# Kernel tuning notes

Measured on AMD Instinct MI355X. Metric: run time of the kernel, lower is better.

The kernel has to match this reference:

```python
import jax, jax.numpy as jnp
import numpy as np

D_MODEL = 1024
NUM_HEADS = 16
HEAD_DIM = D_MODEL // NUM_HEADS


def setup_inputs() -> dict:
    key = jax.random.key(0)
    ks = jax.random.split(key, 7)
    B, S = 4, 2048
    scale = 1.0 / np.sqrt(D_MODEL)
    x = jax.random.normal(ks[0], (B, S, D_MODEL), dtype=jnp.float32)
    Wq = jax.random.normal(ks[1], (D_MODEL, D_MODEL), dtype=jnp.float32) * scale
    Wk = jax.random.normal(ks[2], (D_MODEL, D_MODEL), dtype=jnp.float32) * scale
    Wv = jax.random.normal(ks[3], (D_MODEL, D_MODEL), dtype=jnp.float32) * scale
    bq = jax.random.normal(ks[4], (D_MODEL,), dtype=jnp.float32) * 0.02
    bk = jax.random.normal(ks[5], (D_MODEL,), dtype=jnp.float32) * 0.02
    bv = jax.random.normal(ks[6], (D_MODEL,), dtype=jnp.float32) * 0.02
    return {"x": x, "Wq": Wq, "bq": bq, "Wk": Wk, "bk": bk, "Wv": Wv, "bv": bv}


def reference(x, Wq, bq, Wk, bk, Wv, bv):
    B, S, _ = x.shape
    # QKV projections (nn.Linear: x @ W^T + b; here W stored as [in, out] already)
    q = x @ Wq + bq
    k = x @ Wk + bk
    v = x @ Wv + bv
    # [B, H, S, Dh]
    def split_heads(t):
        return t.reshape(B, S, NUM_HEADS, HEAD_DIM).transpose(0, 2, 1, 3)
    q, k, v = split_heads(q), split_heads(k), split_heads(v)
    # NOTE: module scales by sqrt(d_model), NOT sqrt(head_dim)
    scores = jnp.einsum("bhqd,bhkd->bhqk", q, k) / jnp.sqrt(jnp.float32(D_MODEL))
    attn = jax.nn.softmax(scores, axis=-1)  # dropout = identity (eval mode)
    out = jnp.einsum("bhqk,bhkd->bhqd", attn, v)
    return out.transpose(0, 2, 1, 3).reshape(B, S, D_MODEL)
```

## Files before the change

kernel.cpp:

```cpp
#include <hip/hip_runtime.h>


typedef __attribute__((ext_vector_type(8))) __bf16 bf16x8;
typedef __attribute__((ext_vector_type(8))) unsigned short ushort8;
typedef __attribute__((ext_vector_type(4))) float floatx4;

#if __has_builtin(__builtin_amdgcn_exp2f)
#define EXP2(x) __builtin_amdgcn_exp2f(x)
#else
#define EXP2(x) __expf((x) * 0.6931471805599453f)
#endif

__device__ __forceinline__ unsigned short f2bf(float f) {
    __bf16 h = (__bf16)f;
    return __builtin_bit_cast(unsigned short, h);
}
__device__ __forceinline__ bf16x8 pack8(floatx4 a, floatx4 b) {
    bf16x8 v = {(__bf16)a[0], (__bf16)a[1], (__bf16)a[2], (__bf16)a[3],
                (__bf16)b[0], (__bf16)b[1], (__bf16)b[2], (__bf16)b[3]};
    return v;
}
__device__ __forceinline__ floatx4 mfma16(bf16x8 a, bf16x8 b, floatx4 c) {
    return __builtin_amdgcn_mfma_f32_16x16x32_bf16(a, b, c, 0, 0, 0);
}
__device__ __forceinline__ int spos(int s) {
    int rk = s & 31;
    return (s & ~31) | (((rk & 15) >> 2) * 8 + ((rk >> 4) << 2) + (rk & 3));
}
__device__ __forceinline__ void glds16(const void* g, void* l) {
    __builtin_amdgcn_global_load_lds(
        (const __attribute__((address_space(1))) unsigned int*)g,
        (__attribute__((address_space(3))) unsigned int*)l, 16, 0, 0);
}

__global__ __launch_bounds__(256) void prep_x(const float* __restrict__ X,
                                              unsigned short* __restrict__ Xb) {
    int i = (blockIdx.x * 256 + threadIdx.x) * 8;
    float4 a = *(const float4*)&X[i];
    float4 b = *(const float4*)&X[i + 4];
    bf16x8 v = {(__bf16)a.x, (__bf16)a.y, (__bf16)a.z, (__bf16)a.w,
                (__bf16)b.x, (__bf16)b.y, (__bf16)b.z, (__bf16)b.w};
    *(bf16x8*)&Xb[i] = v;
}

__global__ __launch_bounds__(256) void prep_wt(
    const float* __restrict__ Wq, const float* __restrict__ Wk,
    const float* __restrict__ Wv,
    unsigned short* __restrict__ WqT, unsigned short* __restrict__ WkT,
    unsigned short* __restrict__ WvT) {
    __shared__ unsigned short Ls[64 * 72];
    const int tid = threadIdx.x, z = blockIdx.z;
    const float* W = (z == 0) ? Wq : (z == 1) ? Wk : Wv;
    unsigned short* WT = (z == 0) ? WqT : (z == 1) ? WkT : WvT;
    const int k0 = (blockIdx.x >> 4) * 64, o0 = (blockIdx.x & 15) * 64;
#pragma unroll
    for (int e = 0; e < 4; ++e) {
        int idx = e * 256 + tid;
        int r = idx >> 4, c = (idx & 15) * 4;
        float4 f = *(const float4*)&W[(size_t)(k0 + r) * 1024 + o0 + c];
        Ls[(c + 0) * 72 + r] = f2bf(f.x);
        Ls[(c + 1) * 72 + r] = f2bf(f.y);
        Ls[(c + 2) * 72 + r] = f2bf(f.z);
        Ls[(c + 3) * 72 + r] = f2bf(f.w);
    }
    __syncthreads();
#pragma unroll
    for (int e = 0; e < 2; ++e) {
        int idx = e * 256 + tid;
        int rr = idx >> 3, ch = (idx & 7) * 8;
        *(ushort8*)&WT[(size_t)(o0 + rr) * 1024 + k0 + ch] =
            *(const ushort8*)&Ls[rr * 72 + ch];
    }
}

__global__ __launch_bounds__(256, 2) void qkv_gemm(
    const unsigned short* __restrict__ Xb,
    const unsigned short* __restrict__ WqT,
    const unsigned short* __restrict__ WkT,
    const unsigned short* __restrict__ WvT,
    const float* __restrict__ bq, const float* __restrict__ bk,
    const float* __restrict__ bv,
    unsigned short* __restrict__ Kh, unsigned short* __restrict__ Vt,
    float* __restrict__ Qs_out) {

    __shared__ __align__(16) unsigned char arena[65536];

    const int tid = threadIdx.x;
    const int w = tid >> 6, lane = tid & 63;
    const int l15 = lane & 15, quad = lane >> 4;
    const int z = blockIdx.z;
    const int tok_base = blockIdx.x * 128, o_base = blockIdx.y * 128;
    const int wr = w >> 1, wc = w & 1;

    const unsigned short* Wsrc = (z == 0) ? WkT : (z == 1) ? WvT : WqT;
    const char* Asrc = (z == 1) ? (const char*)(Wsrc + (size_t)o_base * 1024)
                                : (const char*)(Xb + (size_t)tok_base * 1024);
    const char* Bsrc = (z == 1) ? (const char*)(Xb + (size_t)tok_base * 1024)
                                : (const char*)(Wsrc + (size_t)o_base * 1024);

    const int coff = (((lane & 7) ^ (lane >> 3)) << 4);
    const char* pa[4];
    const char* pb[4];
    unsigned char* la[4];
    unsigned char* lb[4];
#pragma unroll
    for (int e = 0; e < 4; ++e) {
        int r = (e * 4 + w) * 8 + (lane >> 3);
        pa[e] = Asrc + (size_t)r * 2048 + coff;
        pb[e] = Bsrc + (size_t)r * 2048 + coff;
        la[e] = arena + (e * 4 + w) * 1024;
        lb[e] = arena + 16384 + (e * 4 + w) * 1024;
    }
    auto stage = [&](int t) {
        int bo = (t & 1) << 15;
#pragma unroll
        for (int e = 0; e < 4; ++e) {
            glds16(pa[e], la[e] + bo);
            glds16(pb[e], lb[e] + bo);
            pa[e] += 128;
            pb[e] += 128;
        }
    };

    const unsigned cq = (unsigned)((quad ^ (l15 & 7)) << 4);
    unsigned offA[4], offB[4];
#pragma unroll
    for (int t = 0; t < 4; ++t) {
        offA[t] = (unsigned)((wr * 64 + t * 16 + l15) * 128) + cq;
        offB[t] = 16384u + (unsigned)((wc * 64 + t * 16 + l15) * 128) + cq;
    }

    floatx4 acc[4][4];
#pragma unroll
    for (int mt = 0; mt < 4; ++mt)
#pragma unroll
        for (int nt = 0; nt < 4; ++nt) acc[mt][nt] = (floatx4){0.f, 0.f, 0.f, 0.f};

    stage(0);

#pragma unroll 1
    for (int t = 0; t < 16; ++t) {
        if (t < 15) {
            stage(t + 1);
            asm volatile("s_waitcnt vmcnt(8)" ::: "memory");
        } else {
            asm volatile("s_waitcnt vmcnt(0)" ::: "memory");
        }
        __builtin_amdgcn_s_barrier();
        const unsigned bsel = (unsigned)((t & 1) << 15);

        __builtin_amdgcn_s_setprio(1);
#pragma unroll
        for (int kc = 0; kc < 2; ++kc) {
            bf16x8 af[4], bfr[4];
#pragma unroll
            for (int mt = 0; mt < 4; ++mt)
                af[mt] = *(const bf16x8*)
                    &arena[(offA[mt] ^ (unsigned)(kc << 6)) ^ bsel];
#pragma unroll
            for (int nt = 0; nt < 4; ++nt)
                bfr[nt] = *(const bf16x8*)
                    &arena[(offB[nt] ^ (unsigned)(kc << 6)) ^ bsel];
#pragma unroll
            for (int mt = 0; mt < 4; ++mt)
#pragma unroll
                for (int nt = 0; nt < 4; ++nt)
                    acc[mt][nt] = mfma16(af[mt], bfr[nt], acc[mt][nt]);
        }
        __builtin_amdgcn_s_setprio(0);

        asm volatile("s_waitcnt lgkmcnt(0)" ::: "memory");
        __builtin_amdgcn_s_barrier();
    }

    if (z == 0) {
#pragma unroll
        for (int nt = 0; nt < 4; ++nt) {
            int col = o_base + wc * 64 + nt * 16 + l15;
            float bia = bk[col];
            int h = col >> 6, dh = col & 63;
#pragma unroll
            for (int mt = 0; mt < 4; ++mt)
#pragma unroll
                for (int r = 0; r < 4; ++r) {
                    int t = tok_base + wr * 64 + mt * 16 + quad * 4 + r;
                    int bb = t >> 11, s = t & 2047;
                    Kh[(((size_t)(bb * 16 + h)) * 2048 + s) * 64 + dh] =
                        f2bf(acc[mt][nt][r] + bia);
                }
        }
    } else if (z == 1) {
#pragma unroll
        for (int mt = 0; mt < 4; ++mt)
#pragma unroll
            for (int r = 0; r < 4; ++r) {
                int o = o_base + wr * 64 + mt * 16 + quad * 4 + r;
                float bia = bv[o];
#pragma unroll
                for (int nt = 0; nt < 4; ++nt) {
                    int t = tok_base + wc * 64 + nt * 16 + l15;
                    int bb = t >> 11, s = t & 2047;
                    Vt[((size_t)(bb * 1024 + o)) * 2048 + spos(s)] =
                        f2bf(acc[mt][nt][r] + bia);
                }
            }
    } else {
        const float QS = 0.03125f * 1.44269504f;
#pragma unroll
        for (int nt = 0; nt < 4; ++nt) {
            int col = o_base + wc * 64 + nt * 16 + l15;
            float bia = bq[col];
#pragma unroll
            for (int mt = 0; mt < 4; ++mt)
#pragma unroll
                for (int r = 0; r < 4; ++r) {
                    int t = tok_base + wr * 64 + mt * 16 + quad * 4 + r;
                    Qs_out[(size_t)t * 1024 + col] = (acc[mt][nt][r] + bia) * QS;
                }
        }
    }
}

__global__ __launch_bounds__(256, 4) void attn_kernel(
    const unsigned short* __restrict__ Kh,
    const unsigned short* __restrict__ Vt,
    float* __restrict__ out) {

    __shared__ __align__(16) unsigned char arena[32768];

    const int tid = threadIdx.x;
    const int w = tid >> 6, lane = tid & 63;
    const int l15 = lane & 15, quad = lane >> 4;
    const int qb = blockIdx.x, h = blockIdx.y, b = blockIdx.z;
    const size_t head_elems = ((size_t)(b * 16 + h)) * 2048 * 64;

    bf16x8 aq[2][2];
#pragma unroll
    for (int g = 0; g < 2; ++g)
#pragma unroll
        for (int kc = 0; kc < 2; ++kc) {
            const float* qp = out +
                (size_t)(b * 2048 + qb * 128 + w * 32 + g * 16 + l15) * 1024 +
                h * 64 + kc * 32 + quad * 8;
            floatx4 x0 = *(const floatx4*)qp;
            floatx4 x1 = *(const floatx4*)(qp + 4);
            aq[g][kc] = pack8(x0, x1);
        }
    __builtin_amdgcn_sched_barrier(0);

    const int coff = (((lane & 7) ^ (lane >> 3)) << 4);
    const char* pk[2];
    const char* pv[2];
    unsigned char* lk[2];
    unsigned char* lv[2];
#pragma unroll
    for (int e = 0; e < 2; ++e) {
        int r = (e * 4 + w) * 8 + (lane >> 3);
        pk[e] = (const char*)Kh + head_elems * 2 + (size_t)r * 128 + coff;
        pv[e] = (const char*)Vt + ((size_t)(b * 1024 + h * 64 + r)) * 4096 + coff;
        lk[e] = arena + (e * 4 + w) * 1024;
        lv[e] = arena + 8192 + (e * 4 + w) * 1024;
    }
    auto stage = [&](int bufsel) {
        int bo = bufsel << 14;
#pragma unroll
        for (int e = 0; e < 2; ++e) {
            glds16(pk[e], lk[e] + bo);
            glds16(pv[e], lv[e] + bo);
            pk[e] += 8192;
            pv[e] += 128;
        }
    };

    unsigned kb[4], vb[4];
#pragma unroll
    for (int t = 0; t < 4; ++t) {
        int rk = t * 16 + l15;
        unsigned sw = (unsigned)((quad ^ (rk & 7)) << 4);
        kb[t] = (unsigned)(rk * 128) + sw;
        vb[t] = 8192u + (unsigned)(rk * 128) + sw;
    }

    const bf16x8 ONES = {(__bf16)1.f, (__bf16)1.f, (__bf16)1.f, (__bf16)1.f,
                         (__bf16)1.f, (__bf16)1.f, (__bf16)1.f, (__bf16)1.f};
    floatx4 lacc[2];
    floatx4 O[2][4];
#pragma unroll
    for (int g = 0; g < 2; ++g) {
        lacc[g] = (floatx4){0.f, 0.f, 0.f, 0.f};
#pragma unroll
        for (int n4 = 0; n4 < 4; ++n4) O[g][n4] = (floatx4){0.f, 0.f, 0.f, 0.f};
    }

    stage(0);

#pragma unroll 1
    for (int kt = 0; kt < 32; ++kt) {
        if (kt < 31) {
            stage((kt + 1) & 1);
            asm volatile("s_waitcnt vmcnt(4)" ::: "memory");
        } else {
            asm volatile("s_waitcnt vmcnt(0)" ::: "memory");
        }
        __builtin_amdgcn_s_barrier();
        const unsigned bsel = (unsigned)((kt & 1) << 14);

        bf16x8 ap[2][2];
#pragma unroll
        for (int kg = 0; kg < 2; ++kg) {
            floatx4 s0[2], s1[2];
            __builtin_amdgcn_s_setprio(1);
#pragma unroll
            for (int mm = 0; mm < 2; ++mm) {
                int m16 = 2 * kg + mm;
                unsigned ka = kb[m16] ^ bsel;
                bf16x8 kf0 = *(const bf16x8*)&arena[ka];
                bf16x8 kf1 = *(const bf16x8*)&arena[ka ^ 64u];
#pragma unroll
                for (int g = 0; g < 2; ++g) {
                    floatx4 a0 = (floatx4){0.f, 0.f, 0.f, 0.f};
                    a0 = mfma16(kf0, aq[g][0], a0);
                    a0 = mfma16(kf1, aq[g][1], a0);
                    if (mm == 0) s0[g] = a0; else s1[g] = a0;
                }
            }
            __builtin_amdgcn_s_setprio(0);
#pragma unroll
            for (int g = 0; g < 2; ++g) {
                floatx4 p0, p1;
#pragma unroll
                for (int r = 0; r < 4; ++r) {
                    p0[r] = EXP2(s0[g][r]);
                    p1[r] = EXP2(s1[g][r]);
                }
                ap[g][kg] = pack8(p0, p1);
                lacc[g] = mfma16(ap[g][kg], ONES, lacc[g]);
            }
        }

        __builtin_amdgcn_s_setprio(1);
#pragma unroll
        for (int n4 = 0; n4 < 4; ++n4)
#pragma unroll
            for (int kg = 0; kg < 2; ++kg) {
                bf16x8 vf = *(const bf16x8*)
                    &arena[(vb[n4] ^ bsel) ^ (unsigned)(kg << 6)];
#pragma unroll
                for (int g = 0; g < 2; ++g)
                    O[g][n4] = mfma16(ap[g][kg], vf, O[g][n4]);
            }
        __builtin_amdgcn_s_setprio(0);

        asm volatile("s_waitcnt lgkmcnt(0)" ::: "memory");
        __builtin_amdgcn_s_barrier();
    }

#pragma unroll
    for (int g = 0; g < 2; ++g)
#pragma unroll
        for (int r = 0; r < 4; ++r) {
            float inv = 1.f / lacc[g][r];
            int srow = qb * 128 + w * 32 + g * 16 + quad * 4 + r;
#pragma unroll
            for (int n4 = 0; n4 < 4; ++n4)
                out[((size_t)(b * 2048 + srow)) * 1024 + h * 64 + n4 * 16 + l15] =
                    O[g][n4][r] * inv;
        }
}

extern "C" void kernel_launch(void* const* d_in, const int* in_sizes, int n_in,
                              void* d_out, int out_size, void* d_ws, size_t ws_size,
                              hipStream_t stream) {
    const float *x, *Wq, *bq, *Wk, *bk, *Wv, *bv;
    x = (const float*)d_in[0];
    if (in_sizes[2] == 1024) {
        Wq = (const float*)d_in[1];  bq = (const float*)d_in[2];
        Wk = (const float*)d_in[3];  bk = (const float*)d_in[4];
        Wv = (const float*)d_in[5];  bv = (const float*)d_in[6];
    } else {
        Wq = (const float*)d_in[1];  Wk = (const float*)d_in[2];
        Wv = (const float*)d_in[3];
        bq = (const float*)d_in[4];  bk = (const float*)d_in[5];
        bv = (const float*)d_in[6];
    }
    float* out = (float*)d_out;

    char* ws = (char*)d_ws;
    unsigned short* Xb  = (unsigned short*)(ws);
    unsigned short* Kh  = (unsigned short*)(ws + (16u << 20));
    unsigned short* Vt  = (unsigned short*)(ws + (32u << 20));
    unsigned short* WqT = (unsigned short*)(ws + (48u << 20));
    unsigned short* WkT = (unsigned short*)(ws + (50u << 20));
    unsigned short* WvT = (unsigned short*)(ws + (52u << 20));

    prep_x<<<4096, 256, 0, stream>>>(x, Xb);
    prep_wt<<<dim3(256, 1, 3), 256, 0, stream>>>(Wq, Wk, Wv, WqT, WkT, WvT);
    qkv_gemm<<<dim3(64, 8, 3), 256, 0, stream>>>(Xb, WqT, WkT, WvT, bq, bk, bv,
                                                 Kh, Vt, out);
    attn_kernel<<<dim3(16, 16, 4), 256, 0, stream>>>(Kh, Vt, out);
}
```

Baseline: 225.4 us.

## Halve QKV GEMM K-tile to fit four blocks per CU and drop swizzle

The QKV projection GEMM now stages 32-wide K slices instead of 64, halving its LDS arena so launch bounds can request four resident blocks per CU. The XOR swizzle on LDS addresses is removed in favour of a plain 64-byte row stride, and explicit lgkmcnt waits before loop-end barriers are dropped in both the GEMM and attention kernels. The aim is more occupancy and less sync overhead. In exchange there are twice as many loop iterations and barriers, and possible LDS bank conflicts from the unswizzled layout.

```diff
diff --git a/kernel.cpp b/kernel.cpp
--- a/kernel.cpp
+++ b/kernel.cpp
@@ -73,7 +73,7 @@
     }
 }
 
-__global__ __launch_bounds__(256, 2) void qkv_gemm(
+__global__ __launch_bounds__(256, 4) void qkv_gemm(
     const unsigned short* __restrict__ Xb,
     const unsigned short* __restrict__ WqT,
     const unsigned short* __restrict__ WkT,
@@ -83,7 +83,7 @@
     unsigned short* __restrict__ Kh, unsigned short* __restrict__ Vt,
     float* __restrict__ Qs_out) {
 
-    __shared__ __align__(16) unsigned char arena[65536];
+    __shared__ __align__(16) unsigned char arena[32768];
 
     const int tid = threadIdx.x;
     const int w = tid >> 6, lane = tid & 63;
@@ -98,36 +98,35 @@
     const char* Bsrc = (z == 1) ? (const char*)(Xb + (size_t)tok_base * 1024)
                                 : (const char*)(Wsrc + (size_t)o_base * 1024);
 
-    const int coff = (((lane & 7) ^ (lane >> 3)) << 4);
-    const char* pa[4];
-    const char* pb[4];
-    unsigned char* la[4];
-    unsigned char* lb[4];
-#pragma unroll
-    for (int e = 0; e < 4; ++e) {
-        int r = (e * 4 + w) * 8 + (lane >> 3);
-        pa[e] = Asrc + (size_t)r * 2048 + coff;
-        pb[e] = Bsrc + (size_t)r * 2048 + coff;
-        la[e] = arena + (e * 4 + w) * 1024;
-        lb[e] = arena + 16384 + (e * 4 + w) * 1024;
-    }
-    auto stage = [&](int t) {
-        int bo = (t & 1) << 15;
-#pragma unroll
-        for (int e = 0; e < 4; ++e) {
+    const char* pa[2];
+    const char* pb[2];
+    unsigned char* la[2];
+    unsigned char* lb[2];
+#pragma unroll
+    for (int e = 0; e < 2; ++e) {
+        int seg = e * 4 + w;
+        size_t roff = (size_t)(seg * 16 + (lane >> 2)) * 2048 + (lane & 3) * 16;
+        pa[e] = Asrc + roff;
+        pb[e] = Bsrc + roff;
+        la[e] = arena + seg * 1024;
+        lb[e] = arena + 8192 + seg * 1024;
+    }
+    auto stage = [&](int buf) {
+        int bo = buf << 14;
+#pragma unroll
+        for (int e = 0; e < 2; ++e) {
             glds16(pa[e], la[e] + bo);
             glds16(pb[e], lb[e] + bo);
-            pa[e] += 128;
-            pb[e] += 128;
+            pa[e] += 64;
+            pb[e] += 64;
         }
     };
 
-    const unsigned cq = (unsigned)((quad ^ (l15 & 7)) << 4);
     unsigned offA[4], offB[4];
 #pragma unroll
     for (int t = 0; t < 4; ++t) {
-        offA[t] = (unsigned)((wr * 64 + t * 16 + l15) * 128) + cq;
-        offB[t] = 16384u + (unsigned)((wc * 64 + t * 16 + l15) * 128) + cq;
+        offA[t] = (unsigned)((wr * 64 + t * 16 + l15) * 64 + quad * 16);
+        offB[t] = 8192u + (unsigned)((wc * 64 + t * 16 + l15) * 64 + quad * 16);
     }
 
     floatx4 acc[4][4];
@@ -139,37 +138,31 @@
     stage(0);
 
 #pragma unroll 1
-    for (int t = 0; t < 16; ++t) {
-        if (t < 15) {
-            stage(t + 1);
-            asm volatile("s_waitcnt vmcnt(8)" ::: "memory");
+    for (int t = 0; t < 32; ++t) {
+        if (t < 31) {
+            stage((t + 1) & 1);
+            asm volatile("s_waitcnt vmcnt(4)" ::: "memory");
         } else {
             asm volatile("s_waitcnt vmcnt(0)" ::: "memory");
         }
         __builtin_amdgcn_s_barrier();
-        const unsigned bsel = (unsigned)((t & 1) << 15);
+        const unsigned bo = (unsigned)((t & 1) << 14);
 
         __builtin_amdgcn_s_setprio(1);
-#pragma unroll
-        for (int kc = 0; kc < 2; ++kc) {
-            bf16x8 af[4], bfr[4];
-#pragma unroll
-            for (int mt = 0; mt < 4; ++mt)
-                af[mt] = *(const bf16x8*)
-                    &arena[(offA[mt] ^ (unsigned)(kc << 6)) ^ bsel];
+        bf16x8 af[4], bfr[4];
+#pragma unroll
+        for (int mt = 0; mt < 4; ++mt)
+            af[mt] = *(const bf16x8*)&arena[offA[mt] + bo];
+#pragma unroll
+        for (int nt = 0; nt < 4; ++nt)
+            bfr[nt] = *(const bf16x8*)&arena[offB[nt] + bo];
+#pragma unroll
+        for (int mt = 0; mt < 4; ++mt)
 #pragma unroll
             for (int nt = 0; nt < 4; ++nt)
-                bfr[nt] = *(const bf16x8*)
-                    &arena[(offB[nt] ^ (unsigned)(kc << 6)) ^ bsel];
-#pragma unroll
-            for (int mt = 0; mt < 4; ++mt)
-#pragma unroll
-                for (int nt = 0; nt < 4; ++nt)
-                    acc[mt][nt] = mfma16(af[mt], bfr[nt], acc[mt][nt]);
-        }
+                acc[mt][nt] = mfma16(af[mt], bfr[nt], acc[mt][nt]);
         __builtin_amdgcn_s_setprio(0);
 
-        asm volatile("s_waitcnt lgkmcnt(0)" ::: "memory");
         __builtin_amdgcn_s_barrier();
     }
 
@@ -351,7 +344,6 @@
             }
         __builtin_amdgcn_s_setprio(0);
 
-        asm volatile("s_waitcnt lgkmcnt(0)" ::: "memory");
         __builtin_amdgcn_s_barrier();
     }
 
```

Measured after the change: 236.6 us. 1.05x slower.
